# Kernel tuning notes

Measured on AMD Instinct MI355X. Metric: run time of the kernel, lower is better.

## Reference

```python
import jax, jax.numpy as jnp
import numpy as np

N, NIN, NOUT = 8192, 512, 512


def setup_inputs() -> dict:
    key = jax.random.key(0)
    k1, k2, k3 = jax.random.split(key, 3)
    H = jax.random.normal(k1, (N, NIN), dtype=jnp.float32)
    adj_matrix = jax.random.uniform(k2, (N, N), dtype=jnp.float32)
    W = jax.random.normal(k3, (NOUT, NIN), dtype=jnp.float32) / np.sqrt(NIN)
    b = jnp.zeros((NOUT,), dtype=jnp.float32)
    return {"H": H, "adj_matrix": adj_matrix, "W": W, "b": b}


def reference(H, adj_matrix, W, b):
    n = adj_matrix.shape[0]
    # adj + I (self-loops)
    A = adj_matrix + jnp.eye(n, dtype=adj_matrix.dtype)
    # column degrees (torch.sum(dim=0))
    deg = jnp.sum(A, axis=0)
    d = deg ** -0.5
    d = jnp.where(jnp.isinf(d), 0.0, d)
    # D^-1/2 A D^-1/2 implemented as elementwise row/col rescale (same math as diag matmuls)
    A = d[:, None] * A * d[None, :]
    # message passing + linear (torch Linear: x @ W.T + b) + tanh
    Hm = A @ H  # [N, nin]
    out = jnp.tanh(Hm @ W.T + b)
    return out
```

## Files before the change

### kernel.cpp

```cpp
#include <hip/hip_runtime.h>
#include <hip/hip_bf16.h>

#define N_NODES 8192
#define N_IN 512
#define N_OUT 512

typedef __bf16 bf16;
typedef __bf16 bf16x4 __attribute__((ext_vector_type(4)));
typedef __bf16 bf16x8 __attribute__((ext_vector_type(8)));
typedef float f32x4 __attribute__((ext_vector_type(4)));

__device__ __forceinline__ void gload16(const void* g, void* l) {
  __builtin_amdgcn_global_load_lds((const __attribute__((address_space(1))) void*)g,
                                   (__attribute__((address_space(3))) void*)l, 16, 0, 0);
}

#define WAITVM(N) asm volatile("s_waitcnt vmcnt(" #N ")" ::: "memory")

__global__ __launch_bounds__(256) void k_colsum_cvt(const float* __restrict__ adj,
                                                    bf16* __restrict__ adjb,
                                                    float* __restrict__ partial) {
  const int tid  = threadIdx.x;
  const int col0 = blockIdx.x * 1024 + tid * 4;
  const int row0 = blockIdx.y * 64;
  float s0 = 0.f, s1 = 0.f, s2 = 0.f, s3 = 0.f;
#pragma unroll 4
  for (int r = 0; r < 64; ++r) {
    const float4 v = *reinterpret_cast<const float4*>(adj + (size_t)(row0 + r) * N_NODES + col0);
    s0 += v.x; s1 += v.y; s2 += v.z; s3 += v.w;
    bf16x4 o = { (bf16)v.x, (bf16)v.y, (bf16)v.z, (bf16)v.w };
    *reinterpret_cast<bf16x4*>(adjb + (size_t)(row0 + r) * N_NODES + col0) = o;
  }
  float4 ps = { s0, s1, s2, s3 };
  *reinterpret_cast<float4*>(partial + (size_t)blockIdx.y * N_NODES + col0) = ps;
}

__global__ __launch_bounds__(256) void k_dvec(const float* __restrict__ partial,
                                              float* __restrict__ dv) {
  const int j = blockIdx.x * 256 + threadIdx.x;
  float s = 1.0f;
#pragma unroll 8
  for (int p = 0; p < 128; ++p) s += partial[(size_t)p * N_NODES + j];
  dv[j] = rsqrtf(s);
}

__global__ __launch_bounds__(256) void k_hst(const float* __restrict__ H,
                                             const float* __restrict__ dv,
                                             bf16* __restrict__ Hst) {
  __shared__ float t[64][65];
  const int tid = threadIdx.x;
  const int j0 = blockIdx.x * 64;
  const int k0 = blockIdx.y * 64;
  const int rr = tid >> 4;
  const int cc = (tid & 15) * 4;
#pragma unroll
  for (int p = 0; p < 4; ++p) {
    const int r = p * 16 + rr;
    const float d = dv[j0 + r];
    float4 v = *reinterpret_cast<const float4*>(H + (size_t)(j0 + r) * N_IN + k0 + cc);
    t[r][cc + 0] = v.x * d; t[r][cc + 1] = v.y * d;
    t[r][cc + 2] = v.z * d; t[r][cc + 3] = v.w * d;
  }
  __syncthreads();
#pragma unroll
  for (int p = 0; p < 4; ++p) {
    const int kr = p * 16 + rr;
    bf16x4 o = { (bf16)t[cc + 0][kr], (bf16)t[cc + 1][kr],
                 (bf16)t[cc + 2][kr], (bf16)t[cc + 3][kr] };
    *reinterpret_cast<bf16x4*>(Hst + (size_t)(k0 + kr) * N_NODES + j0 + cc) = o;
  }
}

__global__ __launch_bounds__(256) void k_wcvt(const float* __restrict__ W, bf16* __restrict__ Wb) {
  const int i = (blockIdx.x * 256 + threadIdx.x) * 4;
  float4 v = *reinterpret_cast<const float4*>(W + i);
  bf16x4 o = { (bf16)v.x, (bf16)v.y, (bf16)v.z, (bf16)v.w };
  *reinterpret_cast<bf16x4*>(Wb + i) = o;
}

template<int KDIM, int EPI>
__global__ __launch_bounds__(256, 1) void k_gemm(
    const bf16* __restrict__ A, const bf16* __restrict__ B,
    const float* __restrict__ dvec, const float* __restrict__ Hf,
    const float* __restrict__ bias, bf16* __restrict__ outb, float* __restrict__ outf) {
  constexpr int NT = KDIM / 64;
  __shared__ __attribute__((aligned(128))) char lds[4 * 32768];

  const int bid = blockIdx.x;
  const int logical = (bid & 7) * 32 + (bid >> 3);
  const int bm0 = (logical >> 2) * 128;
  const int bn0 = (logical & 3) * 128;

  const int tid = threadIdx.x;
  const int wid = tid >> 6;
  const int lane = tid & 63;
  const int wr = wid & 1, wc = wid >> 1;

  const int srow = tid >> 3;
  const int scol = ((tid & 7) ^ (srow & 7)) << 3;
  const size_t a_src = (size_t)(bm0 + srow) * KDIM + scol;
  const size_t b_src = (size_t)(bn0 + srow) * KDIM + scol;

  const int frow = lane & 15;
  const int fk = lane >> 4;
  const int swz = (lane & 7) << 4;
  const int a_row_byte = (wr * 64 + frow) * 128;
  const int b_row_byte = 16384 + (wc * 64 + frow) * 128;

  f32x4 acc[4][4] = {};

  auto stage = [&](int t) {
    const int buf = t & 3;
    char* lbase = lds + buf * 32768;
    const bf16* ag = A + a_src + (size_t)t * 64;
    const bf16* bg = B + b_src + (size_t)t * 64;
#pragma unroll
    for (int ch = 0; ch < 4; ++ch) {
      gload16(ag + (size_t)(ch * 32) * KDIM, lbase + ch * 4096 + wid * 1024);
      gload16(bg + (size_t)(ch * 32) * KDIM, lbase + 16384 + ch * 4096 + wid * 1024);
    }
  };

  auto compute = [&](int t) {
    const char* lbase = lds + (t & 3) * 32768;
#pragma unroll
    for (int kk = 0; kk < 2; ++kk) {
      const int colb = (kk * 64 + fk * 16) ^ swz;
      bf16x8 av[4], bv[4];
#pragma unroll
      for (int m = 0; m < 4; ++m)
        av[m] = *reinterpret_cast<const bf16x8*>(lbase + a_row_byte + m * 2048 + colb);
#pragma unroll
      for (int n = 0; n < 4; ++n)
        bv[n] = *reinterpret_cast<const bf16x8*>(lbase + b_row_byte + n * 2048 + colb);
#pragma unroll
      for (int m = 0; m < 4; ++m)
#pragma unroll
        for (int n = 0; n < 4; ++n)
          acc[m][n] = __builtin_amdgcn_mfma_f32_16x16x32_bf16(av[m], bv[n], acc[m][n], 0, 0, 0);
    }
  };

  stage(0); stage(1); stage(2);
  for (int t = 0; t < NT; ++t) {
    if (t + 3 < NT) stage(t + 3);
    const int ahead = NT - 1 - t;
    if (ahead >= 3)      WAITVM(24);
    else if (ahead == 2) WAITVM(16);
    else if (ahead == 1) WAITVM(8);
    else                 WAITVM(0);
    __builtin_amdgcn_s_barrier();
    asm volatile("" ::: "memory");
    compute(t);
    asm volatile("" ::: "memory");
    __builtin_amdgcn_s_barrier();
  }

#pragma unroll
  for (int m = 0; m < 4; ++m) {
#pragma unroll
    for (int j = 0; j < 4; ++j) {
      const int grow = bm0 + wr * 64 + m * 16 + (lane >> 4) * 4 + j;
      if constexpr (EPI == 0) {
        const float d = dvec[grow];
        const float d2 = d * d;
        const float* hrow = Hf + (size_t)grow * N_IN;
        bf16* orow = outb + (size_t)grow * N_IN;
#pragma unroll
        for (int n = 0; n < 4; ++n) {
          const int gcol = bn0 + wc * 64 + n * 16 + (lane & 15);
          orow[gcol] = (bf16)(d * acc[m][n][j] + d2 * hrow[gcol]);
        }
      } else {
        float* orow = outf + (size_t)grow * N_OUT;
#pragma unroll
        for (int n = 0; n < 4; ++n) {
          const int gcol = bn0 + wc * 64 + n * 16 + (lane & 15);
          float v = acc[m][n][j] + bias[gcol];
          v = fminf(fmaxf(v, -15.f), 15.f);
          const float e = __expf(2.f * v);
          orow[gcol] = (e - 1.f) / (e + 1.f);
        }
      }
    }
  }
}

extern "C" void kernel_launch(void* const* d_in, const int* in_sizes, int n_in,
                              void* d_out, int out_size, void* d_ws, size_t ws_size,
                              hipStream_t stream) {
  const float* H   = (const float*)d_in[0];
  const float* adj = (const float*)d_in[1];
  const float* W   = (const float*)d_in[2];
  const float* b   = (const float*)d_in[3];
  float* out = (float*)d_out;
  char* ws = (char*)d_ws;

  bf16*  adjb = (bf16*)(ws);
  bf16*  Hst  = (bf16*)(ws + 134217728);
  bf16*  Hm   = (bf16*)(ws + 142606336);
  bf16*  Wb   = (bf16*)(ws + 150994944);
  float* part = (float*)(ws + 151519232);
  float* dv   = (float*)(ws + 155713536);

  k_colsum_cvt<<<dim3(8, 128), 256, 0, stream>>>(adj, adjb, part);
  k_dvec<<<32, 256, 0, stream>>>(part, dv);
  k_hst<<<dim3(128, 8), 256, 0, stream>>>(H, dv, Hst);
  k_wcvt<<<256, 256, 0, stream>>>(W, Wb);
  k_gemm<8192, 0><<<256, 256, 0, stream>>>(adjb, Hst, dv, H, nullptr, Hm, nullptr);
  k_gemm<512, 1><<<256, 256, 0, stream>>>(Hm, Wb, nullptr, nullptr, b, nullptr, out);
}
```

Before: 198.5 us.

## Split-K the big aggregation GEMM into two halves with a reduction kernel

The N×N by N×512 GEMM now splits K into two halves, launching 512 blocks instead of 256 so more CUs are busy (256 tiles underfill the MI355X). The LDS pipeline shrinks from four stages to two with launch_bounds(256,2), allowing two blocks per CU. Partial fp32 results go to a new workspace buffer, and a separate reduction kernel applies the degree scaling and self-loop term and converts to bf16. This costs 32 MB of extra fp32 partial writes and reads, plus an extra launch and shallower prefetch.

Result: slower. 208.3 us (+4.9%).

```diff
diff --git a/kernel.cpp b/kernel.cpp
--- a/kernel.cpp
+++ b/kernel.cpp
@@ -78,18 +78,21 @@
   *reinterpret_cast<bf16x4*>(Wb + i) = o;
 }
 
-template<int KDIM, int EPI>
-__global__ __launch_bounds__(256, 1) void k_gemm(
+template<int KDIM, int NSPLIT, int EPI>
+__global__ __launch_bounds__(256, 2) void k_gemm(
     const bf16* __restrict__ A, const bf16* __restrict__ B,
-    const float* __restrict__ dvec, const float* __restrict__ Hf,
-    const float* __restrict__ bias, bf16* __restrict__ outb, float* __restrict__ outf) {
-  constexpr int NT = KDIM / 64;
-  __shared__ __attribute__((aligned(128))) char lds[4 * 32768];
+    const float* __restrict__ bias, float* __restrict__ outf) {
+  constexpr int KSEG = KDIM / NSPLIT;
+  constexpr int NT = KSEG / 64;
+  constexpr int NBLK = 256 * NSPLIT;
+  __shared__ __attribute__((aligned(128))) char lds[2 * 32768];
 
   const int bid = blockIdx.x;
-  const int logical = (bid & 7) * 32 + (bid >> 3);
-  const int bm0 = (logical >> 2) * 128;
-  const int bn0 = (logical & 3) * 128;
+  const int logical = (bid & 7) * (NBLK / 8) + (bid >> 3);
+  const int split = logical & (NSPLIT - 1);
+  const int tile = logical / NSPLIT;
+  const int bm0 = (tile >> 2) * 128;
+  const int bn0 = (tile & 3) * 128;
 
   const int tid = threadIdx.x;
   const int wid = tid >> 6;
@@ -98,8 +101,8 @@
 
   const int srow = tid >> 3;
   const int scol = ((tid & 7) ^ (srow & 7)) << 3;
-  const size_t a_src = (size_t)(bm0 + srow) * KDIM + scol;
-  const size_t b_src = (size_t)(bn0 + srow) * KDIM + scol;
+  const size_t a_src = (size_t)(bm0 + srow) * KDIM + (size_t)split * KSEG + scol;
+  const size_t b_src = (size_t)(bn0 + srow) * KDIM + (size_t)split * KSEG + scol;
 
   const int frow = lane & 15;
   const int fk = lane >> 4;
@@ -110,8 +113,7 @@
   f32x4 acc[4][4] = {};
 
   auto stage = [&](int t) {
-    const int buf = t & 3;
-    char* lbase = lds + buf * 32768;
+    char* lbase = lds + (t & 1) * 32768;
     const bf16* ag = A + a_src + (size_t)t * 64;
     const bf16* bg = B + b_src + (size_t)t * 64;
 #pragma unroll
@@ -122,7 +124,7 @@
   };
 
   auto compute = [&](int t) {
-    const char* lbase = lds + (t & 3) * 32768;
+    const char* lbase = lds + (t & 1) * 32768;
 #pragma unroll
     for (int kk = 0; kk < 2; ++kk) {
       const int colb = (kk * 64 + fk * 16) ^ swz;
@@ -141,35 +143,32 @@
     }
   };
 
-  stage(0); stage(1); stage(2);
-  for (int t = 0; t < NT; ++t) {
-    if (t + 3 < NT) stage(t + 3);
-    const int ahead = NT - 1 - t;
-    if (ahead >= 3)      WAITVM(24);
-    else if (ahead == 2) WAITVM(16);
-    else if (ahead == 1) WAITVM(8);
-    else                 WAITVM(0);
+  stage(0);
+#pragma unroll 1
+  for (int t = 0; t < NT - 1; ++t) {
+    stage(t + 1);
+    WAITVM(8);
     __builtin_amdgcn_s_barrier();
     asm volatile("" ::: "memory");
     compute(t);
     asm volatile("" ::: "memory");
     __builtin_amdgcn_s_barrier();
   }
+  WAITVM(0);
+  __builtin_amdgcn_s_barrier();
+  compute(NT - 1);
 
 #pragma unroll
   for (int m = 0; m < 4; ++m) {
 #pragma unroll
     for (int j = 0; j < 4; ++j) {
       const int grow = bm0 + wr * 64 + m * 16 + (lane >> 4) * 4 + j;
-      if constexpr (EPI == 0) {
-        const float d = dvec[grow];
-        const float d2 = d * d;
-        const float* hrow = Hf + (size_t)grow * N_IN;
-        bf16* orow = outb + (size_t)grow * N_IN;
+      if constexpr (EPI == 2) {
+        float* prow = outf + (size_t)split * ((size_t)N_NODES * N_IN) + (size_t)grow * N_IN;
 #pragma unroll
         for (int n = 0; n < 4; ++n) {
           const int gcol = bn0 + wc * 64 + n * 16 + (lane & 15);
-          orow[gcol] = (bf16)(d * acc[m][n][j] + d2 * hrow[gcol]);
+          prow[gcol] = acc[m][n][j];
         }
       } else {
         float* orow = outf + (size_t)grow * N_OUT;
@@ -186,6 +185,26 @@
   }
 }
 
+__global__ __launch_bounds__(256) void k_red(const float* __restrict__ P,
+                                             const float* __restrict__ H,
+                                             const float* __restrict__ dv,
+                                             bf16* __restrict__ Hm) {
+  const int t = blockIdx.x * 256 + threadIdx.x;
+  const int row = t >> 7;
+  const int col = (t & 127) << 2;
+  const size_t off = (size_t)row * N_IN + col;
+  const float d = dv[row];
+  const float d2 = d * d;
+  const float4 p0 = *reinterpret_cast<const float4*>(P + off);
+  const float4 p1 = *reinterpret_cast<const float4*>(P + (size_t)N_NODES * N_IN + off);
+  const float4 h  = *reinterpret_cast<const float4*>(H + off);
+  bf16x4 o = { (bf16)(d * (p0.x + p1.x) + d2 * h.x),
+               (bf16)(d * (p0.y + p1.y) + d2 * h.y),
+               (bf16)(d * (p0.z + p1.z) + d2 * h.z),
+               (bf16)(d * (p0.w + p1.w) + d2 * h.w) };
+  *reinterpret_cast<bf16x4*>(Hm + off) = o;
+}
+
 extern "C" void kernel_launch(void* const* d_in, const int* in_sizes, int n_in,
                               void* d_out, int out_size, void* d_ws, size_t ws_size,
                               hipStream_t stream) {
@@ -202,11 +221,13 @@
   bf16*  Wb   = (bf16*)(ws + 150994944);
   float* part = (float*)(ws + 151519232);
   float* dv   = (float*)(ws + 155713536);
+  float* P    = (float*)(ws + 155746304);
 
   k_colsum_cvt<<<dim3(8, 128), 256, 0, stream>>>(adj, adjb, part);
   k_dvec<<<32, 256, 0, stream>>>(part, dv);
   k_hst<<<dim3(128, 8), 256, 0, stream>>>(H, dv, Hst);
   k_wcvt<<<256, 256, 0, stream>>>(W, Wb);
-  k_gemm<8192, 0><<<256, 256, 0, stream>>>(adjb, Hst, dv, H, nullptr, Hm, nullptr);
-  k_gemm<512, 1><<<256, 256, 0, stream>>>(Hm, Wb, nullptr, nullptr, b, nullptr, out);
-}
+  k_gemm<8192, 2, 2><<<512, 256, 0, stream>>>(adjb, Hst, nullptr, P);
+  k_red<<<4096, 256, 0, stream>>>(P, H, dv, Hm);
+  k_gemm<512, 1, 1><<<256, 256, 0, stream>>>(Hm, Wb, b, out);
+}
```
